# Kernel tuning notes

Hardware: AMD Instinct MI355X
Metric: run time of the kernel (lower is better)

The kernel has to match this reference:

```python
import jax, jax.numpy as jnp
import numpy as np

N_NODES = 50000
N_EDGES = 800000
D_IN = 64
D_HID = 64
N_GRAPHS = 64


def setup_inputs() -> dict:
    key = jax.random.key(0)
    ks = jax.random.split(key, 10)
    x = jax.random.normal(ks[0], (N_NODES, D_IN), dtype=jnp.float32)
    edge_index = jax.random.randint(ks[1], (2, N_EDGES), 0, N_NODES, dtype=jnp.int64)
    batch = jnp.sort(jax.random.randint(ks[2], (N_NODES,), 0, N_GRAPHS, dtype=jnp.int64))
    s1 = 1.0 / np.sqrt(D_IN)
    s2 = 1.0 / np.sqrt(D_HID)
    W1 = jax.random.uniform(ks[3], (D_IN, D_HID), jnp.float32, -s1, s1)
    b1 = jnp.zeros((D_HID,), jnp.float32)
    W2 = jax.random.uniform(ks[4], (D_HID, D_HID), jnp.float32, -s2, s2)
    b2 = jnp.zeros((D_HID,), jnp.float32)
    W3 = jax.random.uniform(ks[5], (D_HID, D_HID), jnp.float32, -s2, s2)
    b3 = jnpp = jnp.zeros((D_HID,), jnp.float32)
    return {"x": x, "edge_index": edge_index, "batch": batch,
            "W1": W1, "b1": b1, "W2": W2, "b2": b2, "W3": W3, "b3": b3}


def _gcn_norm(edge_index, num_nodes):
    # add self-loops, then symmetric normalization deg^-1/2 A_hat deg^-1/2
    loop = jnp.arange(num_nodes, dtype=edge_index.dtype)
    row = jnp.concatenate([edge_index[0], loop])  # source
    col = jnp.concatenate([edge_index[1], loop])  # target (aggregation index)
    deg = jax.ops.segment_sum(jnp.ones_like(col, dtype=jnp.float32), col,
                              num_segments=num_nodes)
    dinv = jnp.where(deg > 0, jax.lax.rsqrt(deg), 0.0)
    norm = dinv[row] * dinv[col]  # [E+N]
    return row, col, norm


def _gcn_conv(x, row, col, norm, W, b, num_nodes):
    h = x @ W                                   # [N, D] small GEMM
    msg = h[row] * norm[:, None]                # edge-wise gather + scale
    out = jax.ops.segment_sum(msg, col, num_segments=num_nodes)  # scatter-add
    return out + b


def reference(x, edge_index, batch, W1, b1, W2, b2, W3, b3):
    n = x.shape[0]
    row, col, norm = _gcn_norm(edge_index, n)
    h = jax.nn.relu(_gcn_conv(x, row, col, norm, W1, b1, n))
    h = jax.nn.relu(_gcn_conv(h, row, col, norm, W2, b2, n))
    h = jax.nn.relu(_gcn_conv(h, row, col, norm, W3, b3, n))
    # global_mean_pool over graphs
    sums = jax.ops.segment_sum(h, batch, num_segments=N_GRAPHS)
    cnt = jax.ops.segment_sum(jnp.ones((n,), jnp.float32), batch,
                              num_segments=N_GRAPHS)
    return sums / jnp.maximum(cnt, 1.0)[:, None]
```

## Files before the change

kernel.cpp:

```cpp
#include <hip/hip_runtime.h>

#define N_NODES   50000
#define N_EDGES   800000
#define DF        64
#define N_GRAPHS  64
#define NPAD      50176

#define ABLK 200
#define AEDG (N_EDGES/ABLK)
#define RSH  9
#define NREG 98
#define RPAD 128
#define CAP  12288

__global__ __launch_bounds__(256)
void k_hist(const int* __restrict__ col, int* __restrict__ H,
            float* __restrict__ pool) {
    __shared__ int h[RPAD];
    const int t = threadIdx.x, b = blockIdx.x;
    if (b == 0)
        for (int i = t; i < N_GRAPHS * DF; i += 256) pool[i] = 0.f;
    if (t < RPAD) h[t] = 0;
    __syncthreads();
    const int e0 = b * AEDG;
    for (int i = t; i < AEDG; i += 256)
        atomicAdd(&h[col[e0 + i] >> RSH], 1);
    __syncthreads();
    if (t < RPAD) H[t * ABLK + b] = h[t];
}

__global__ __launch_bounds__(256)
void k_scanH(const int* __restrict__ H, int* __restrict__ O,
             int* __restrict__ T) {
    __shared__ int s[256];
    const int t = threadIdx.x, r = blockIdx.x;
    int v = (t < ABLK) ? H[r * ABLK + t] : 0;
    s[t] = v; __syncthreads();
    #pragma unroll
    for (int off = 1; off < 256; off <<= 1) {
        int x = (t >= off) ? s[t - off] : 0;
        __syncthreads();
        s[t] += x;
        __syncthreads();
    }
    if (t < ABLK) O[r * ABLK + t] = s[t] - v;
    if (t == 255) T[r] = s[255];
}

__global__ __launch_bounds__(256)
void k_bin(const int* __restrict__ row, const int* __restrict__ col,
           const int* __restrict__ O, const int* __restrict__ T,
           unsigned* __restrict__ staging) {
    __shared__ int cur[RPAD];
    __shared__ int rs[RPAD];
    const int t = threadIdx.x, b = blockIdx.x;
    int v = 0;
    if (t < RPAD) { v = T[t]; rs[t] = v; }
    __syncthreads();
    #pragma unroll
    for (int off = 1; off < RPAD; off <<= 1) {
        int x = 0;
        if (t < RPAD && t >= off) x = rs[t - off];
        __syncthreads();
        if (t < RPAD) rs[t] += x;
        __syncthreads();
    }
    if (t < RPAD) cur[t] = O[t * ABLK + b] + (rs[t] - v);
    __syncthreads();
    const int e0 = b * AEDG;
    for (int i = t; i < AEDG; i += 256) {
        int c = col[e0 + i];
        int rr = row[e0 + i];
        int slot = atomicAdd(&cur[c >> RSH], 1);
        staging[slot] = ((unsigned)c << 16) | (unsigned)rr;
    }
}

__global__ __launch_bounds__(512)
void k_csr(const unsigned* __restrict__ staging, const int* __restrict__ T,
           int* __restrict__ offs, float* __restrict__ dinv,
           unsigned* __restrict__ epack) {
    __shared__ int hist[512];
    __shared__ int cur[512];
    __shared__ unsigned img[CAP];
    __shared__ int rs[RPAD];
    __shared__ int sh_s0, sh_s1;
    const int t = threadIdx.x, r = blockIdx.x;
    int v = 0;
    if (t < RPAD) { v = T[t]; rs[t] = v; }
    __syncthreads();
    #pragma unroll
    for (int off = 1; off < RPAD; off <<= 1) {
        int x = 0;
        if (t < RPAD && t >= off) x = rs[t - off];
        __syncthreads();
        if (t < RPAD) rs[t] += x;
        __syncthreads();
    }
    if (t == r) { sh_s0 = rs[t] - v; sh_s1 = rs[t]; }
    hist[t] = 0;
    __syncthreads();
    const int s0 = sh_s0, s1 = sh_s1;
    for (int i = s0 + t; i < s1; i += 512) {
        int ln = (int)(staging[i] >> 16) - (r << RSH);
        atomicAdd(&hist[ln], 1);
    }
    __syncthreads();
    int myc = hist[t];
    #pragma unroll
    for (int off = 1; off < 512; off <<= 1) {
        int x = (t >= off) ? hist[t - off] : 0;
        __syncthreads();
        hist[t] += x;
        __syncthreads();
    }
    int excl = hist[t] - myc;
    int n = (r << RSH) + t;
    offs[n] = s0 + excl;
    if (n < N_NODES) dinv[n] = rsqrtf((float)(myc + 1));
    cur[t] = excl;
    __syncthreads();
    for (int i = s0 + t; i < s1; i += 512) {
        unsigned p = staging[i];
        int ln = (int)(p >> 16) - (r << RSH);
        unsigned rr = p & 0xFFFFu;
        unsigned pk = rr | ((unsigned)ln << 16);
        int slot = atomicAdd(&cur[ln], 1);
        if (slot < CAP) img[slot] = pk;
        else           epack[s0 + slot] = pk;
    }
    __syncthreads();
    int cnt = s1 - s0; if (cnt > CAP) cnt = CAP;
    for (int j = t; j < cnt; j += 512) epack[s0 + j] = img[j];
}

#define FB_ROWS 64
#define LDX 68
#define ECAP 2048

__global__ __launch_bounds__(512, 4)
void k_fused(const int* __restrict__ offs, const unsigned* __restrict__ epack,
             const float* __restrict__ dinv, const float* __restrict__ h,
             const float* __restrict__ W, const float* __restrict__ bias,
             float* __restrict__ out, const int* __restrict__ batch,
             float* __restrict__ pool) {
    __shared__ float  XsT[DF][LDX];
    __shared__ float  Ws[DF][DF];
    __shared__ float2 ew_l[ECAP];
    __shared__ int    s_offs[FB_ROWS + 1];
    __shared__ float  sh_dinv[FB_ROWS];
    __shared__ float  plocal[4 * DF];
    __shared__ int    sh_batch[FB_ROWS];

    const int t = threadIdx.x;
    const int row0 = blockIdx.x * FB_ROWS;

    for (int idx = t * 4; idx < DF * DF; idx += 512 * 4) {
        float4 w = *(const float4*)&W[idx];
        Ws[idx >> 6][(idx & 63) + 0] = w.x;
        Ws[idx >> 6][(idx & 63) + 1] = w.y;
        Ws[idx >> 6][(idx & 63) + 2] = w.z;
        Ws[idx >> 6][(idx & 63) + 3] = w.w;
    }
    if (t <= FB_ROWS) s_offs[t] = offs[row0 + t];
    if (t < FB_ROWS) {
        int n = row0 + t;
        sh_dinv[t] = (n < N_NODES) ? dinv[n] : 0.f;
    }
    if (pool) {
        if (t < 4 * DF) plocal[t] = 0.f;
        if (t < FB_ROWS) {
            int n = row0 + t;
            sh_batch[t] = batch[n < N_NODES ? n : N_NODES - 1];
        }
    }
    __syncthreads();

    const int eb  = s_offs[0];
    const int cnt = s_offs[FB_ROWS] - eb;
    const int lim = cnt < ECAP ? cnt : ECAP;
    for (int i = t; i < lim; i += 512) {
        unsigned src = epack[eb + i] & 0xFFFFu;
        ew_l[i] = make_float2(dinv[src], __uint_as_float(src));
    }
    __syncthreads();

    const int wv = t >> 6;
    const int l  = t & 63;
    const int ng = l >> 4;
    const int q4 = (l & 15) << 2;

    for (int set = 0; set < 2; ++set) {
        const int r = (wv << 3) + (set << 2) + ng;
        const int n = row0 + r;
        const float dc = sh_dinv[r];
        const unsigned hn = (n < N_NODES) ? (unsigned)n : 0u;

        float4 acc;
        {
            float4 xv = *(const float4*)&h[(hn << 6) + q4];
            acc.x = dc * xv.x; acc.y = dc * xv.y;
            acc.z = dc * xv.z; acc.w = dc * xv.w;
        }

        int s        = s_offs[r]     - eb;
        const int s1 = s_offs[r + 1] - eb;
        while (s < s1) {
            unsigned srcs[8]; float wgts[8];
            #pragma unroll
            for (int k = 0; k < 8; ++k) {
                const int li = s + k;
                unsigned sr = hn; float wg = 0.f;
                if (li < s1) {
                    if (li < ECAP) {
                        float2 ew = ew_l[li];
                        wg = ew.x; sr = __float_as_uint(ew.y);
                    } else {
                        sr = epack[eb + li] & 0xFFFFu;
                        wg = dinv[sr];
                    }
                }
                srcs[k] = sr; wgts[k] = wg;
            }
            float4 v[8];
            #pragma unroll
            for (int k = 0; k < 8; ++k)
                v[k] = *(const float4*)&h[(srcs[k] << 6) + q4];
            #pragma unroll
            for (int k = 0; k < 8; ++k) {
                acc.x += wgts[k] * v[k].x; acc.y += wgts[k] * v[k].y;
                acc.z += wgts[k] * v[k].z; acc.w += wgts[k] * v[k].w;
            }
            s += 8;
        }

        XsT[q4 + 0][r] = acc.x * dc;
        XsT[q4 + 1][r] = acc.y * dc;
        XsT[q4 + 2][r] = acc.z * dc;
        XsT[q4 + 3][r] = acc.w * dc;
    }
    __syncthreads();

    const int i = (t & 15) * 4;
    const int j = (t >> 4) * 2;
    float acc[4][2] = {};
    #pragma unroll 8
    for (int k = 0; k < DF; ++k) {
        float4 xv = *(const float4*)&XsT[k][i];
        float2 wvv = *(const float2*)&Ws[k][j];
        acc[0][0] += xv.x * wvv.x; acc[0][1] += xv.x * wvv.y;
        acc[1][0] += xv.y * wvv.x; acc[1][1] += xv.y * wvv.y;
        acc[2][0] += xv.z * wvv.x; acc[2][1] += xv.z * wvv.y;
        acc[3][0] += xv.w * wvv.x; acc[3][1] += xv.w * wvv.y;
    }
    const float bx = bias[j], by = bias[j + 1];

    if (!pool) {
        #pragma unroll
        for (int u = 0; u < 4; ++u) {
            int gr = row0 + i + u;
            if (gr < N_NODES) {
                float ox = acc[u][0] + bx;
                float oy = acc[u][1] + by;
                ox = ox > 0.f ? ox : 0.f;
                oy = oy > 0.f ? oy : 0.f;
                *(float2*)&out[gr * DF + j] = make_float2(ox, oy);
            }
        }
    } else {
        const int g0 = sh_batch[0];
        const int span = sh_batch[FB_ROWS - 1] - g0 + 1;
        if (span <= 4) {
            #pragma unroll
            for (int u = 0; u < 4; ++u) {
                int gr = row0 + i + u;
                if (gr < N_NODES) {
                    float ox = acc[u][0] + bx;
                    float oy = acc[u][1] + by;
                    ox = ox > 0.f ? ox : 0.f;
                    oy = oy > 0.f ? oy : 0.f;
                    int gl = sh_batch[i + u] - g0;
                    atomicAdd(&plocal[gl * DF + j],     ox);
                    atomicAdd(&plocal[gl * DF + j + 1], oy);
                }
            }
            __syncthreads();
            for (int idx = t; idx < span * DF; idx += 512)
                atomicAdd(&pool[g0 * DF + idx], plocal[idx]);
        } else {
            #pragma unroll
            for (int u = 0; u < 4; ++u) {
                int gr = row0 + i + u;
                if (gr < N_NODES) {
                    float ox = acc[u][0] + bx;
                    float oy = acc[u][1] + by;
                    ox = ox > 0.f ? ox : 0.f;
                    oy = oy > 0.f ? oy : 0.f;
                    int gg = sh_batch[i + u];
                    atomicAdd(&pool[gg * DF + j],     ox);
                    atomicAdd(&pool[gg * DF + j + 1], oy);
                }
            }
        }
    }
}

__device__ __forceinline__ int lb(const int* a, int n, int key) {
    int lo = 0, hi = n;
    while (lo < hi) { int m = (lo + hi) >> 1; if (a[m] < key) lo = m + 1; else hi = m; }
    return lo;
}

__global__ void k_div(const float* __restrict__ pool, const int* __restrict__ batch,
                      float* __restrict__ out) {
    int idx = blockIdx.x * blockDim.x + threadIdx.x;
    if (idx < N_GRAPHS * DF) {
        int g = idx >> 6;
        int c = lb(batch, N_NODES, g + 1) - lb(batch, N_NODES, g);
        out[idx] = pool[idx] / fmaxf((float)c, 1.0f);
    }
}


extern "C" void kernel_launch(void* const* d_in, const int* in_sizes, int n_in,
                              void* d_out, int out_size, void* d_ws, size_t ws_size,
                              hipStream_t stream) {
    const float* x     = (const float*)d_in[0];
    const int*   ei    = (const int*)d_in[1];
    const int*   batch = (const int*)d_in[2];
    const float* W1    = (const float*)d_in[3];
    const float* b1    = (const float*)d_in[4];
    const float* W2    = (const float*)d_in[5];
    const float* b2    = (const float*)d_in[6];
    const float* W3    = (const float*)d_in[7];
    const float* b3    = (const float*)d_in[8];
    float* out = (float*)d_out;

    const int* row = ei;
    const int* col = ei + N_EDGES;

    char* wsb = (char*)d_ws;
    float*    pool    = (float*)wsb;
    int*      H       = (int*)(pool + N_GRAPHS * DF);
    int*      O       = H + RPAD * ABLK;
    int*      T       = O + RPAD * ABLK;
    int*      offs    = T + RPAD;
    unsigned* epack   = (unsigned*)(offs + NPAD);
    unsigned* staging = epack + N_EDGES;
    float*    dinv    = (float*)(staging + N_EDGES);
    float*    bufA    = dinv + NPAD;
    float*    bufB    = bufA + N_NODES * DF;

    const int nblk_F = (N_NODES + FB_ROWS - 1) / FB_ROWS;

    k_hist<<<ABLK, 256, 0, stream>>>(col, H, pool);
    k_scanH<<<RPAD, 256, 0, stream>>>(H, O, T);
    k_bin<<<ABLK, 256, 0, stream>>>(row, col, O, T, staging);
    k_csr<<<NREG, 512, 0, stream>>>(staging, T, offs, dinv, epack);

    k_fused<<<nblk_F, 512, 0, stream>>>(offs, epack, dinv, x,    W1, b1, bufA,
                                        nullptr, nullptr);
    k_fused<<<nblk_F, 512, 0, stream>>>(offs, epack, dinv, bufA, W2, b2, bufB,
                                        nullptr, nullptr);
    k_fused<<<nblk_F, 512, 0, stream>>>(offs, epack, dinv, bufB, W3, b3, nullptr,
                                        batch, pool);

    k_div<<<(N_GRAPHS * DF + 255) / 256, 256, 0, stream>>>(pool, batch, out);
}
```

Before: 258.5 us.

## Pre-scale node features by source dinv to drop per-edge weight loads

Adds a pre-pass kernel that multiplies input features by dinv, and makes each layer write its output already scaled by dinv. The aggregation can then sum the gathered rows without a per-edge weight. The shared edge cache shrinks from float2 (weight plus index) to 16-bit indices, and launch bounds ask for 8 blocks per CU instead of 4. The cost is an extra elementwise kernel and a full pass over x, plus possible register pressure from the higher occupancy target.

```diff
diff --git a/kernel.cpp b/kernel.cpp
--- a/kernel.cpp
+++ b/kernel.cpp
@@ -134,21 +134,33 @@
     for (int j = t; j < cnt; j += 512) epack[s0 + j] = img[j];
 }
 
+__global__ __launch_bounds__(256)
+void k_scale(const float* __restrict__ x, const float* __restrict__ dinv,
+             float* __restrict__ hs) {
+    int i = blockIdx.x * blockDim.x + threadIdx.x;
+    if (i < N_NODES * DF / 4) {
+        int n = (i * 4) >> 6;
+        float s = dinv[n];
+        float4 v = ((const float4*)x)[i];
+        v.x *= s; v.y *= s; v.z *= s; v.w *= s;
+        ((float4*)hs)[i] = v;
+    }
+}
+
 #define FB_ROWS 64
 #define LDX 68
 #define ECAP 2048
 
-__global__ __launch_bounds__(512, 4)
+__global__ __launch_bounds__(512, 8)
 void k_fused(const int* __restrict__ offs, const unsigned* __restrict__ epack,
-             const float* __restrict__ dinv, const float* __restrict__ h,
+             const float* __restrict__ dinv, const float* __restrict__ hs,
              const float* __restrict__ W, const float* __restrict__ bias,
              float* __restrict__ out, const int* __restrict__ batch,
              float* __restrict__ pool) {
     __shared__ float  XsT[DF][LDX];
     __shared__ float  Ws[DF][DF];
-    __shared__ float2 ew_l[ECAP];
+    __shared__ unsigned short es_l[ECAP];
     __shared__ int    s_offs[FB_ROWS + 1];
-    __shared__ float  sh_dinv[FB_ROWS];
     __shared__ float  plocal[4 * DF];
     __shared__ int    sh_batch[FB_ROWS];
 
@@ -163,10 +175,6 @@
         Ws[idx >> 6][(idx & 63) + 3] = w.w;
     }
     if (t <= FB_ROWS) s_offs[t] = offs[row0 + t];
-    if (t < FB_ROWS) {
-        int n = row0 + t;
-        sh_dinv[t] = (n < N_NODES) ? dinv[n] : 0.f;
-    }
     if (pool) {
         if (t < 4 * DF) plocal[t] = 0.f;
         if (t < FB_ROWS) {
@@ -179,10 +187,8 @@
     const int eb  = s_offs[0];
     const int cnt = s_offs[FB_ROWS] - eb;
     const int lim = cnt < ECAP ? cnt : ECAP;
-    for (int i = t; i < lim; i += 512) {
-        unsigned src = epack[eb + i] & 0xFFFFu;
-        ew_l[i] = make_float2(dinv[src], __uint_as_float(src));
-    }
+    for (int i = t; i < lim; i += 512)
+        es_l[i] = (unsigned short)(epack[eb + i] & 0xFFFFu);
     __syncthreads();
 
     const int wv = t >> 6;
@@ -193,43 +199,34 @@
     for (int set = 0; set < 2; ++set) {
         const int r = (wv << 3) + (set << 2) + ng;
         const int n = row0 + r;
-        const float dc = sh_dinv[r];
+        const float dc = (n < N_NODES) ? dinv[n] : 0.f;
         const unsigned hn = (n < N_NODES) ? (unsigned)n : 0u;
 
-        float4 acc;
-        {
-            float4 xv = *(const float4*)&h[(hn << 6) + q4];
-            acc.x = dc * xv.x; acc.y = dc * xv.y;
-            acc.z = dc * xv.z; acc.w = dc * xv.w;
-        }
+        float4 acc = *(const float4*)&hs[(hn << 6) + q4];
 
         int s        = s_offs[r]     - eb;
         const int s1 = s_offs[r + 1] - eb;
         while (s < s1) {
-            unsigned srcs[8]; float wgts[8];
+            unsigned srcs[8];
             #pragma unroll
             for (int k = 0; k < 8; ++k) {
                 const int li = s + k;
-                unsigned sr = hn; float wg = 0.f;
-                if (li < s1) {
-                    if (li < ECAP) {
-                        float2 ew = ew_l[li];
-                        wg = ew.x; sr = __float_as_uint(ew.y);
-                    } else {
-                        sr = epack[eb + li] & 0xFFFFu;
-                        wg = dinv[sr];
-                    }
-                }
-                srcs[k] = sr; wgts[k] = wg;
+                unsigned sr = hn;
+                if (li < s1)
+                    sr = (li < ECAP) ? (unsigned)es_l[li]
+                                     : (epack[eb + li] & 0xFFFFu);
+                srcs[k] = (li < s1) ? sr : hn;
             }
             float4 v[8];
             #pragma unroll
             for (int k = 0; k < 8; ++k)
-                v[k] = *(const float4*)&h[(srcs[k] << 6) + q4];
+                v[k] = *(const float4*)&hs[(srcs[k] << 6) + q4];
             #pragma unroll
             for (int k = 0; k < 8; ++k) {
-                acc.x += wgts[k] * v[k].x; acc.y += wgts[k] * v[k].y;
-                acc.z += wgts[k] * v[k].z; acc.w += wgts[k] * v[k].w;
+                const int li = s + k;
+                const float m = (li < s1) ? 1.f : 0.f;
+                acc.x += m * v[k].x; acc.y += m * v[k].y;
+                acc.z += m * v[k].z; acc.w += m * v[k].w;
             }
             s += 8;
         }
@@ -260,11 +257,12 @@
         for (int u = 0; u < 4; ++u) {
             int gr = row0 + i + u;
             if (gr < N_NODES) {
+                float sc = dinv[gr];
                 float ox = acc[u][0] + bx;
                 float oy = acc[u][1] + by;
                 ox = ox > 0.f ? ox : 0.f;
                 oy = oy > 0.f ? oy : 0.f;
-                *(float2*)&out[gr * DF + j] = make_float2(ox, oy);
+                *(float2*)&out[gr * DF + j] = make_float2(ox * sc, oy * sc);
             }
         }
     } else {
@@ -352,13 +350,16 @@
     float*    bufB    = bufA + N_NODES * DF;
 
     const int nblk_F = (N_NODES + FB_ROWS - 1) / FB_ROWS;
+    const int nblk_S = (N_NODES * DF / 4 + 255) / 256;
 
     k_hist<<<ABLK, 256, 0, stream>>>(col, H, pool);
     k_scanH<<<RPAD, 256, 0, stream>>>(H, O, T);
     k_bin<<<ABLK, 256, 0, stream>>>(row, col, O, T, staging);
     k_csr<<<NREG, 512, 0, stream>>>(staging, T, offs, dinv, epack);
 
-    k_fused<<<nblk_F, 512, 0, stream>>>(offs, epack, dinv, x,    W1, b1, bufA,
+    k_scale<<<nblk_S, 256, 0, stream>>>(x, dinv, bufB);
+
+    k_fused<<<nblk_F, 512, 0, stream>>>(offs, epack, dinv, bufB, W1, b1, bufA,
                                         nullptr, nullptr);
     k_fused<<<nblk_F, 512, 0, stream>>>(offs, epack, dinv, bufA, W2, b2, bufB,
                                         nullptr, nullptr);
```

Result: faster. 245.1 us (-5.2%).
